# Kernel tuning notes

Measured on AMD Instinct MI355X. Metric: run time of the kernel, lower is better.

The kernel has to match this reference:

```python
import jax, jax.numpy as jnp
import numpy as np

OC, IC, KH, KW = 256, 128, 3, 3          # conv_weights_shape
S, R, Q = 16, 16, 16                      # n_subspaces, rank_transformations, rank_subspace
CTX = 256
HD, WD = OC * KH, IC * KW                 # dynamic_weights_shape = [768, 384]
ASYM = 1e-3
B = 32


def _make_index():
    # Faithful vectorization of DynamicConv2DMobius._create_index for the
    # non-inverted case (HD > WD): block_id = bi*nbj + bj over 3x3 tiles of the
    # [HD, WD] grid; tile goes to (out = block_id % OC, in = block_id // OC).
    base = np.arange(HD * WD).reshape(HD, WD)
    nbi, nbj = HD // KH, WD // KW          # == OC, IC here
    blocks = base.reshape(nbi, KH, nbj, KW).transpose(0, 2, 1, 3).reshape(nbi * nbj, KH, KW)
    # index[o, i] = blocks[i*OC + o]
    index = blocks.reshape(IC, OC, KH, KW).transpose(1, 0, 2, 3)
    return index.reshape(-1).astype(np.int32)  # flat gather map: conv.flat = dw.flat[idx]


def setup_inputs() -> dict:
    key = jax.random.key(0)
    ks = jax.random.split(key, 12)
    bconv_bound = 1.0 / np.sqrt(IC * KH * KW)
    return {
        "x": jax.random.normal(ks[0], (B, IC, 64, 64), jnp.float32),
        "context": jax.random.normal(ks[1], (B, CTX), jnp.float32),
        "W_mob": jax.random.normal(ks[2], (CTX, S, R, 8), jnp.float32) * 0.05,
        "z": jax.random.normal(ks[3], (S, R, 2), jnp.float32),
        "A_re": jax.random.normal(ks[4], (S, R, Q), jnp.float32) * 0.1,
        "A_im": jax.random.normal(ks[5], (S, R, Q), jnp.float32) * 0.1,
        "U": jax.random.normal(ks[6], (S, HD, Q), jnp.float32) * 0.05,
        "V": jax.random.normal(ks[7], (S, Q, WD), jnp.float32) * 0.05,
        "bias_dw": jax.random.uniform(ks[8], (HD, WD), jnp.float32, -ASYM, ASYM),
        "bias_conv": jax.random.uniform(ks[9], (OC,), jnp.float32, -bconv_bound, bconv_bound),
        "pad_val": jax.random.normal(ks[10], (1,), jnp.float32) * 1e-3,
        "offset_val": jax.random.normal(ks[11], (1,), jnp.float32) * 1e-3,
        "dw_index": jnp.asarray(_make_index()),
    }


def _forward(x, context, W_mob, z, A_re, A_im, U, V, bias_dw, bias_conv,
             pad_val, offset_val, dw_index):
    b = x.shape[0]
    # --- TensorComposerMobius: context -> per-sample Mobius coeffs -> low-rank weights
    m = jnp.einsum('bc,csrk->bsrk', context, W_mob)            # [B,S,R,8]
    a_re, a_im, b_re, b_im, c_re, c_im, d_re, d_im = [m[..., i] for i in range(8)]
    z_re, z_im = z[..., 0], z[..., 1]                           # [S,R]
    num_re = a_re * z_re - a_im * z_im + b_re
    num_im = a_re * z_im + a_im * z_re + b_im
    den_re = c_re * z_re - c_im * z_im + d_re
    den_im = c_re * z_im + c_im * z_re + d_im
    den2 = den_re * den_re + den_im * den_im + ASYM             # asymmetry regularizer
    w_re = (num_re * den_re + num_im * den_im) / den2
    w_im = (num_im * den_re - num_re * den_im) / den2
    s = jnp.einsum('bsr,srq->bsq', w_re, A_re) + jnp.einsum('bsr,srq->bsq', w_im, A_im)
    dw = jnp.einsum('bsq,shq,sqw->bhw', s, U, V)                # [B, 768, 384]
    dw = dw + bias_dw[None]                                     # bias_dynamic_weights_lib
    # --- block-gather into conv weight layout (torch.take with shifted index)
    conv_w = jnp.take(dw.reshape(b, -1), dw_index, axis=1).reshape(b, OC, IC, KH, KW)
    # --- dynamic padding value + dynamic offset
    xo = x + offset_val[0]
    hp, wp = x.shape[2] + 2, x.shape[3] + 2                     # padding [1,1,1,1]
    xp = jnp.full((b, IC, hp, wp), pad_val[0], x.dtype).at[:, :, 1:-1, 1:-1].set(xo)
    # --- per-sample conv2d (batched weights)
    def conv_one(xi, wi):
        return jax.lax.conv_general_dilated(
            xi[None], wi, window_strides=(1, 1), padding='VALID',
            rhs_dilation=(1, 1), dimension_numbers=('NCHW', 'OIHW', 'NCHW'))[0]
    out = jax.vmap(conv_one)(xp, conv_w)                        # [B, OC, 64, 64]
    return out + bias_conv[None, :, None, None]


def reference(x, context, W_mob, z, A_re, A_im, U, V, bias_dw, bias_conv,
              pad_val, offset_val, dw_index):
    return _forward(x, context, W_mob, z, A_re, A_im, U, V, bias_dw, bias_conv,
                    pad_val, offset_val, dw_index)
```

## Files before the change

kernel.cpp:

```cpp
#include <hip/hip_runtime.h>
#include <hip/hip_bf16.h>

typedef __attribute__((ext_vector_type(8))) short short8;
typedef __attribute__((ext_vector_type(4))) float f32x4;
typedef unsigned short u16;

#define B_      32
#define IC_     128
#define OC_     256
#define HD_     768
#define WD_     384
#define CTX_    256

static __device__ __forceinline__ u16 f2bf(float f) {
    union { float f; unsigned u; } x; x.f = f;
    unsigned r = x.u + 0x7FFFu + ((x.u >> 16) & 1u);
    return (u16)(r >> 16);
}

static __device__ __forceinline__ void glds16(const void* g, void* l) {
    __builtin_amdgcn_global_load_lds(
        (const __attribute__((address_space(1))) unsigned*)g,
        (__attribute__((address_space(3))) unsigned*)l, 16, 0, 0);
}

#define BARRIER() asm volatile("s_barrier" ::: "memory")
template <int N> static __device__ __forceinline__ void waitvm() {
    if constexpr (N == 0)      asm volatile("s_waitcnt vmcnt(0)" ::: "memory");
    else if constexpr (N == 4) asm volatile("s_waitcnt vmcnt(4)" ::: "memory");
    else if constexpr (N == 9) asm volatile("s_waitcnt vmcnt(9)" ::: "memory");
}

__global__ __launch_bounds__(256) void k1_mobius(
    const float* __restrict__ ctx, const float* __restrict__ Wm,
    const float* __restrict__ z, const float* __restrict__ Are,
    const float* __restrict__ Aim, float* __restrict__ sc) {
    int b = blockIdx.x, t = threadIdx.x;
    __shared__ float lctx[CTX_];
    __shared__ float lwre[256], lwim[256];
    lctx[t] = ctx[b * CTX_ + t];
    __syncthreads();
    float m0=0,m1=0,m2=0,m3=0,m4=0,m5=0,m6=0,m7=0;
    const float4* wp4 = (const float4*)Wm + (size_t)t * 2;
    #pragma unroll 4
    for (int c = 0; c < CTX_; ++c) {
        float4 w0 = wp4[(size_t)c * 512];
        float4 w1 = wp4[(size_t)c * 512 + 1];
        float cv = lctx[c];
        m0 += cv*w0.x; m1 += cv*w0.y; m2 += cv*w0.z; m3 += cv*w0.w;
        m4 += cv*w1.x; m5 += cv*w1.y; m6 += cv*w1.z; m7 += cv*w1.w;
    }
    float zre = z[t*2], zim = z[t*2+1];
    float nre = m0*zre - m1*zim + m2;
    float nim = m0*zim + m1*zre + m3;
    float dre = m4*zre - m5*zim + m6;
    float dim_ = m4*zim + m5*zre + m7;
    float den2 = dre*dre + dim_*dim_ + 1e-3f;
    lwre[t] = (nre*dre + nim*dim_) / den2;
    lwim[t] = (nim*dre - nre*dim_) / den2;
    __syncthreads();
    int s = t >> 4, q = t & 15;
    float acc = 0.f;
    #pragma unroll
    for (int r2 = 0; r2 < 16; ++r2) {
        int sr = s*16 + r2;
        acc += lwre[sr]*Are[sr*16 + q] + lwim[sr]*Aim[sr*16 + q];
    }
    sc[b*256 + t] = acc;
}

__global__ __launch_bounds__(256) void k2_pad(
    const float* __restrict__ x, const float* __restrict__ padv,
    const float* __restrict__ offv, u16* __restrict__ xp) {
    int yy = blockIdx.x, b = blockIdx.y, t = threadIdx.x;
    __shared__ u16 lds[64 * 136];
    float off = offv[0];
    u16 pb = f2bf(padv[0]);
    unsigned pp = (unsigned)pb | ((unsigned)pb << 16);
    int4 padvec = make_int4((int)pp, (int)pp, (int)pp, (int)pp);
    u16* row = xp + (size_t)(b * 66 + yy) * (66 * 128);
    if (yy == 0 || yy == 65) {
        for (int c = t; c < 1056; c += 256)
            *(int4*)(row + c * 8) = padvec;
        return;
    }
    int y = yy - 1;
    const float* xin = x + (size_t)b * 524288 + (size_t)y * 64;
    for (int id = t; id < 8192; id += 256) {
        int i = id >> 6, xx = id & 63;
        lds[xx * 136 + i] = f2bf(xin[(size_t)i * 4096 + xx] + off);
    }
    __syncthreads();
    for (int c = t; c < 1056; c += 256) {
        int e = c * 8, xx = e >> 7, i0 = e & 127;
        int4 v;
        if (xx == 0 || xx == 65) v = padvec;
        else v = *(const int4*)(lds + (xx - 1) * 136 + i0);
        *(int4*)(row + e) = v;
    }
}

__global__ __launch_bounds__(256) void k3_prep(
    const float* __restrict__ U, const float* __restrict__ V,
    u16* __restrict__ Ucat, float* __restrict__ Vt) {
    int id = blockIdx.x * 256 + threadIdx.x;
    if (id < 768 * 256) {
        int h = id >> 8, k = id & 255;
        int s = k >> 4, q = k & 15;
        Ucat[id] = f2bf(U[((size_t)s * HD_ + h) * 16 + q]);
    } else {
        int id2 = id - 768 * 256;
        int w = id2 >> 8, k = id2 & 255;
        Vt[id2] = V[(size_t)k * WD_ + w];
    }
}

__global__ __launch_bounds__(256, 2) void k4_dw(
    const u16* __restrict__ Ucat, const float* __restrict__ Vt,
    const float* __restrict__ sc, const float* __restrict__ bias_dw,
    u16* __restrict__ cw2) {
    int mt = blockIdx.x, khkw = blockIdx.y, b = blockIdx.z;
    int kh = khkw / 3, kw = khkw - kh * 3;
    int t = threadIdx.x;
    __shared__ __align__(16) u16 Al[128 * 40];
    __shared__ __align__(16) u16 Bl[128 * 40];
    __shared__ float scl[256];
    scl[t] = sc[b * 256 + t];
    f32x4 acc[4][4] = {};
    int wid = t >> 6, l = t & 63;
    int wm = wid >> 1, wn = wid & 1;
    int lr = l & 15, lg = l >> 4;
    int bi0 = mt * 128;
    for (int kc = 0; kc < 8; ++kc) {
        __syncthreads();
        #pragma unroll
        for (int it = 0; it < 2; ++it) {
            int cid = t + it * 256;
            int g = cid & 3, rr = cid >> 2;
            int4 v = *(const int4*)(Ucat + (size_t)((bi0 + rr) * 3 + kh) * 256 + kc * 32 + g * 8);
            *(int4*)(Al + rr * 40 + g * 8) = v;
        }
        #pragma unroll
        for (int it = 0; it < 4; ++it) {
            int cid = t + it * 256;
            int q = cid & 7, rr = cid >> 3;
            int kb = kc * 32 + q * 4;
            float4 v = *(const float4*)(Vt + (size_t)(rr * 3 + kw) * 256 + kb);
            ushort4 p;
            p.x = f2bf(v.x * scl[kb]);
            p.y = f2bf(v.y * scl[kb + 1]);
            p.z = f2bf(v.z * scl[kb + 2]);
            p.w = f2bf(v.w * scl[kb + 3]);
            *(ushort4*)(Bl + rr * 40 + q * 4) = p;
        }
        __syncthreads();
        short8 a[4];
        #pragma unroll
        for (int fm = 0; fm < 4; ++fm)
            a[fm] = *(const short8*)(Al + (wm * 64 + fm * 16 + lr) * 40 + lg * 8);
        #pragma unroll
        for (int fn = 0; fn < 4; ++fn) {
            short8 bb = *(const short8*)(Bl + (wn * 64 + fn * 16 + lr) * 40 + lg * 8);
            #pragma unroll
            for (int fm = 0; fm < 4; ++fm)
                acc[fm][fn] = __builtin_amdgcn_mfma_f32_16x16x32_bf16(a[fm], bb, acc[fm][fn], 0, 0, 0);
        }
    }
    u16* cwb = cw2 + (size_t)b * 294912;
    #pragma unroll
    for (int fm = 0; fm < 4; ++fm) {
        int i2 = mt * 8 + wm * 4 + fm;
        int B0 = bi0 + wm * 64 + fm * 16 + lg * 4;
        #pragma unroll
        for (int fn = 0; fn < 4; ++fn) {
            int bjj = wn * 64 + fn * 16 + lr;
            int wcol = bjj * 3 + kw;
            float v0 = acc[fm][fn][0] + bias_dw[(B0 + 0) * 3 * 384 + kh * 384 + wcol];
            float v2 = acc[fm][fn][2] + bias_dw[(B0 + 2) * 3 * 384 + kh * 384 + wcol];
            unsigned pe = (unsigned)f2bf(v0) | ((unsigned)f2bf(v2) << 16);
            size_t base = ((size_t)(khkw * 16 + i2) * 256);
            *(unsigned*)(cwb + (base + bjj) * 8 + 2 * lg) = pe;
            float v1 = acc[fm][fn][1] + bias_dw[(B0 + 1) * 3 * 384 + kh * 384 + wcol];
            float v3 = acc[fm][fn][3] + bias_dw[(B0 + 3) * 3 * 384 + kh * 384 + wcol];
            unsigned po = (unsigned)f2bf(v1) | ((unsigned)f2bf(v3) << 16);
            *(unsigned*)(cwb + (base + bjj + 128) * 8 + 2 * lg) = po;
        }
    }
}

static __device__ __forceinline__ void stage_W(
    const u16* cwb, int khkw, int ic, u16* wl, int t) {
    const u16* slice = cwb + ((size_t)(khkw * 16 + ic * 4) * 256) * 8;
    int wbase = t & ~63;
    #pragma unroll
    for (int it = 0; it < 4; ++it) {
        int cid = it * 256 + t;
        glds16(slice + (size_t)cid * 8, wl + (size_t)(it * 256 + wbase) * 8);
    }
}

static __device__ __forceinline__ void stage_X(
    const u16* xpb, int ic, int y0, u16* xl, int t) {
    int wbase = t & ~63;
    #pragma unroll
    for (int it = 0; it < 5; ++it) {
        int cid = it * 256 + t;
        const u16* g;
        if (cid < 1056) {
            int n = cid ^ ((cid >> 3) & 7);
            int gq = (n >= 792) ? 3 : (n >= 528) ? 2 : (n >= 264) ? 1 : 0;
            int rem = n - gq * 264;
            int r = (rem * 993) >> 16;
            int c = rem - r * 66;
            g = xpb + ((size_t)(y0 + r) * 66 + c) * 128 + ic * 32 + gq * 8;
        } else {
            g = xpb;
        }
        glds16(g, xl + (size_t)(it * 256 + wbase) * 8);
    }
}

__global__ __launch_bounds__(256, 2) void k6_conv(
    const u16* __restrict__ xp, const u16* __restrict__ cw2,
    const float* __restrict__ bias_conv, float* __restrict__ out) {
    int f = blockIdx.x;
    int xcd = f & 7, sub = f >> 3;
    int b = xcd * 4 + (sub >> 5);
    int nt = sub & 31;
    int t = threadIdx.x;
    int y0 = nt * 2;
    __shared__ __align__(16) u16 Wl[2][1024 * 8];
    __shared__ __align__(16) u16 Xl[2][1280 * 8];
    f32x4 acc[4][8] = {};
    int wid = t >> 6, l = t & 63, lr = l & 15, lg = l >> 4;
    const u16* xpb = xp + (size_t)b * (66 * 66 * 128);
    const u16* cwb = cw2 + (size_t)b * 294912;

    stage_X(xpb, 0, y0, Xl[0], t);
    stage_W(cwb, 0, 0, Wl[0], t);
    waitvm<0>();
    BARRIER();

    #pragma unroll
    for (int ic = 0; ic < 4; ++ic) {
        #pragma unroll
        for (int khkw = 0; khkw < 9; ++khkw) {
            const int s = ic * 9 + khkw;
            const int kh = khkw / 3, kw = khkw - kh * 3;
            if (khkw == 8 && ic < 3)
                stage_X(xpb, ic + 1, y0, Xl[(ic + 1) & 1], t);
            if (s + 1 < 36) {
                const int nk = (s + 1) % 9, nic = (s + 1) / 9;
                stage_W(cwb, nk, nic, Wl[(s + 1) & 1], t);
            }
            if (s == 35) waitvm<0>();
            else if (khkw == 8) waitvm<9>();
            else waitvm<4>();
            BARRIER();
            const u16* wl = Wl[s & 1];
            const u16* xl = Xl[ic & 1];
            short8 a[4];
            #pragma unroll
            for (int fm = 0; fm < 4; ++fm) {
                int o = wid * 64 + fm * 16 + lr;
                a[fm] = *(const short8*)(wl + (size_t)(lg * 256 + o) * 8);
            }
            __builtin_amdgcn_s_setprio(1);
            #pragma unroll
            for (int fn = 0; fn < 8; ++fn) {
                int r = (fn >> 2) + kh, c = (fn & 3) * 16 + lr + kw;
                int n = lg * 264 + r * 66 + c;
                int m = n ^ ((n >> 3) & 7);
                short8 bb = *(const short8*)(xl + (size_t)m * 8);
                #pragma unroll
                for (int fm = 0; fm < 4; ++fm)
                    acc[fm][fn] = __builtin_amdgcn_mfma_f32_16x16x32_bf16(a[fm], bb, acc[fm][fn], 0, 0, 0);
            }
            __builtin_amdgcn_s_setprio(0);
            if (s != 35) BARRIER();
        }
    }
    #pragma unroll
    for (int fm = 0; fm < 4; ++fm)
        #pragma unroll
        for (int fn = 0; fn < 8; ++fn) {
            int y = y0 + (fn >> 2);
            int xb = (fn & 3) * 16 + lr;
            #pragma unroll
            for (int j = 0; j < 4; ++j) {
                int o = wid * 64 + fm * 16 + lg * 4 + j;
                out[(((size_t)b * 256 + o) * 64 + y) * 64 + xb] = acc[fm][fn][j] + bias_conv[o];
            }
        }
}

extern "C" void kernel_launch(void* const* d_in, const int* in_sizes, int n_in,
                              void* d_out, int out_size, void* d_ws, size_t ws_size,
                              hipStream_t stream) {
    const float* x     = (const float*)d_in[0];
    const float* ctx   = (const float*)d_in[1];
    const float* Wm    = (const float*)d_in[2];
    const float* z     = (const float*)d_in[3];
    const float* Are   = (const float*)d_in[4];
    const float* Aim   = (const float*)d_in[5];
    const float* U     = (const float*)d_in[6];
    const float* V     = (const float*)d_in[7];
    const float* bdw   = (const float*)d_in[8];
    const float* bconv = (const float*)d_in[9];
    const float* padv  = (const float*)d_in[10];
    const float* offv  = (const float*)d_in[11];
    float* out = (float*)d_out;
    char* ws = (char*)d_ws;

    u16*   xp   = (u16*)(ws);
    u16*   cw2  = (u16*)(ws + 35684352);
    u16*   Ucat = (u16*)(ws + 54558720);
    float* Vt   = (float*)(ws + 54951936);
    float* sc   = (float*)(ws + 55345152);

    k1_mobius<<<32, 256, 0, stream>>>(ctx, Wm, z, Are, Aim, sc);
    k2_pad<<<dim3(66, 32), 256, 0, stream>>>(x, padv, offv, xp);
    k3_prep<<<1152, 256, 0, stream>>>(U, V, Ucat, Vt);
    k4_dw<<<dim3(2, 9, 32), 256, 0, stream>>>(Ucat, Vt, sc, bdw, cw2);
    k6_conv<<<1024, 256, 0, stream>>>(xp, cw2, bconv, out);
}
```

Measured before the change: 350.0 us.

## Load conv weights directly into registers and merge preprocessing kernels into one launch

The conv kernel stops staging weight slices through LDS with double buffering. Each lane now loads its MFMA A-fragments straight from global memory into a two-deep register ring, prefetched two steps ahead, which removes one LDS buffer and most per-step barriers. Barriers and vmcnt waits now happen only when the X tile changes, once per input-channel group. Separately, the mobius, pad and prep kernels are fused into one launch split by block index, saving launch overhead; in exchange the weight loads become uncoalesced 16-byte global reads per lane and register pressure rises.

```diff
diff --git a/kernel.cpp b/kernel.cpp
--- a/kernel.cpp
+++ b/kernel.cpp
@@ -25,93 +25,91 @@
 }
 
 #define BARRIER() asm volatile("s_barrier" ::: "memory")
-template <int N> static __device__ __forceinline__ void waitvm() {
-    if constexpr (N == 0)      asm volatile("s_waitcnt vmcnt(0)" ::: "memory");
-    else if constexpr (N == 4) asm volatile("s_waitcnt vmcnt(4)" ::: "memory");
-    else if constexpr (N == 9) asm volatile("s_waitcnt vmcnt(9)" ::: "memory");
-}
-
-__global__ __launch_bounds__(256) void k1_mobius(
+static __device__ __forceinline__ void waitvm0() {
+    asm volatile("s_waitcnt vmcnt(0)" ::: "memory");
+}
+
+__global__ __launch_bounds__(256) void k_pre(
     const float* __restrict__ ctx, const float* __restrict__ Wm,
     const float* __restrict__ z, const float* __restrict__ Are,
-    const float* __restrict__ Aim, float* __restrict__ sc) {
-    int b = blockIdx.x, t = threadIdx.x;
-    __shared__ float lctx[CTX_];
-    __shared__ float lwre[256], lwim[256];
-    lctx[t] = ctx[b * CTX_ + t];
-    __syncthreads();
-    float m0=0,m1=0,m2=0,m3=0,m4=0,m5=0,m6=0,m7=0;
-    const float4* wp4 = (const float4*)Wm + (size_t)t * 2;
-    #pragma unroll 4
-    for (int c = 0; c < CTX_; ++c) {
-        float4 w0 = wp4[(size_t)c * 512];
-        float4 w1 = wp4[(size_t)c * 512 + 1];
-        float cv = lctx[c];
-        m0 += cv*w0.x; m1 += cv*w0.y; m2 += cv*w0.z; m3 += cv*w0.w;
-        m4 += cv*w1.x; m5 += cv*w1.y; m6 += cv*w1.z; m7 += cv*w1.w;
-    }
-    float zre = z[t*2], zim = z[t*2+1];
-    float nre = m0*zre - m1*zim + m2;
-    float nim = m0*zim + m1*zre + m3;
-    float dre = m4*zre - m5*zim + m6;
-    float dim_ = m4*zim + m5*zre + m7;
-    float den2 = dre*dre + dim_*dim_ + 1e-3f;
-    lwre[t] = (nre*dre + nim*dim_) / den2;
-    lwim[t] = (nim*dre - nre*dim_) / den2;
-    __syncthreads();
-    int s = t >> 4, q = t & 15;
-    float acc = 0.f;
-    #pragma unroll
-    for (int r2 = 0; r2 < 16; ++r2) {
-        int sr = s*16 + r2;
-        acc += lwre[sr]*Are[sr*16 + q] + lwim[sr]*Aim[sr*16 + q];
-    }
-    sc[b*256 + t] = acc;
-}
-
-__global__ __launch_bounds__(256) void k2_pad(
-    const float* __restrict__ x, const float* __restrict__ padv,
-    const float* __restrict__ offv, u16* __restrict__ xp) {
-    int yy = blockIdx.x, b = blockIdx.y, t = threadIdx.x;
-    __shared__ u16 lds[64 * 136];
-    float off = offv[0];
-    u16 pb = f2bf(padv[0]);
-    unsigned pp = (unsigned)pb | ((unsigned)pb << 16);
-    int4 padvec = make_int4((int)pp, (int)pp, (int)pp, (int)pp);
-    u16* row = xp + (size_t)(b * 66 + yy) * (66 * 128);
-    if (yy == 0 || yy == 65) {
-        for (int c = t; c < 1056; c += 256)
-            *(int4*)(row + c * 8) = padvec;
-        return;
-    }
-    int y = yy - 1;
-    const float* xin = x + (size_t)b * 524288 + (size_t)y * 64;
-    for (int id = t; id < 8192; id += 256) {
-        int i = id >> 6, xx = id & 63;
-        lds[xx * 136 + i] = f2bf(xin[(size_t)i * 4096 + xx] + off);
-    }
-    __syncthreads();
-    for (int c = t; c < 1056; c += 256) {
-        int e = c * 8, xx = e >> 7, i0 = e & 127;
-        int4 v;
-        if (xx == 0 || xx == 65) v = padvec;
-        else v = *(const int4*)(lds + (xx - 1) * 136 + i0);
-        *(int4*)(row + e) = v;
-    }
-}
-
-__global__ __launch_bounds__(256) void k3_prep(
+    const float* __restrict__ Aim, const float* __restrict__ x,
+    const float* __restrict__ padv, const float* __restrict__ offv,
     const float* __restrict__ U, const float* __restrict__ V,
+    float* __restrict__ sc, u16* __restrict__ xp,
     u16* __restrict__ Ucat, float* __restrict__ Vt) {
-    int id = blockIdx.x * 256 + threadIdx.x;
-    if (id < 768 * 256) {
-        int h = id >> 8, k = id & 255;
-        int s = k >> 4, q = k & 15;
-        Ucat[id] = f2bf(U[((size_t)s * HD_ + h) * 16 + q]);
+    int bid = blockIdx.x, t = threadIdx.x;
+    if (bid < 32) {
+        int b = bid;
+        __shared__ float lctx[CTX_];
+        __shared__ float lwre[256], lwim[256];
+        lctx[t] = ctx[b * CTX_ + t];
+        __syncthreads();
+        float m0=0,m1=0,m2=0,m3=0,m4=0,m5=0,m6=0,m7=0;
+        const float4* wp4 = (const float4*)Wm + (size_t)t * 2;
+        #pragma unroll 4
+        for (int c = 0; c < CTX_; ++c) {
+            float4 w0 = wp4[(size_t)c * 512];
+            float4 w1 = wp4[(size_t)c * 512 + 1];
+            float cv = lctx[c];
+            m0 += cv*w0.x; m1 += cv*w0.y; m2 += cv*w0.z; m3 += cv*w0.w;
+            m4 += cv*w1.x; m5 += cv*w1.y; m6 += cv*w1.z; m7 += cv*w1.w;
+        }
+        float zre = z[t*2], zim = z[t*2+1];
+        float nre = m0*zre - m1*zim + m2;
+        float nim = m0*zim + m1*zre + m3;
+        float dre = m4*zre - m5*zim + m6;
+        float dim_ = m4*zim + m5*zre + m7;
+        float den2 = dre*dre + dim_*dim_ + 1e-3f;
+        lwre[t] = (nre*dre + nim*dim_) / den2;
+        lwim[t] = (nim*dre - nre*dim_) / den2;
+        __syncthreads();
+        int s = t >> 4, q = t & 15;
+        float acc = 0.f;
+        #pragma unroll
+        for (int r2 = 0; r2 < 16; ++r2) {
+            int sr = s*16 + r2;
+            acc += lwre[sr]*Are[sr*16 + q] + lwim[sr]*Aim[sr*16 + q];
+        }
+        sc[b*256 + t] = acc;
+    } else if (bid < 2144) {
+        int pb_ = bid - 32;
+        int yy = pb_ % 66, b = pb_ / 66;
+        __shared__ u16 lds[64 * 136];
+        float off = offv[0];
+        u16 pb = f2bf(padv[0]);
+        unsigned pp = (unsigned)pb | ((unsigned)pb << 16);
+        int4 padvec = make_int4((int)pp, (int)pp, (int)pp, (int)pp);
+        u16* row = xp + (size_t)(b * 66 + yy) * (66 * 128);
+        if (yy == 0 || yy == 65) {
+            for (int c = t; c < 1056; c += 256)
+                *(int4*)(row + c * 8) = padvec;
+            return;
+        }
+        int y = yy - 1;
+        const float* xin = x + (size_t)b * 524288 + (size_t)y * 64;
+        for (int id = t; id < 8192; id += 256) {
+            int i = id >> 6, xx = id & 63;
+            lds[xx * 136 + i] = f2bf(xin[(size_t)i * 4096 + xx] + off);
+        }
+        __syncthreads();
+        for (int c = t; c < 1056; c += 256) {
+            int e = c * 8, xx = e >> 7, i0 = e & 127;
+            int4 v;
+            if (xx == 0 || xx == 65) v = padvec;
+            else v = *(const int4*)(lds + (xx - 1) * 136 + i0);
+            *(int4*)(row + e) = v;
+        }
     } else {
-        int id2 = id - 768 * 256;
-        int w = id2 >> 8, k = id2 & 255;
-        Vt[id2] = V[(size_t)k * WD_ + w];
+        int id = (bid - 2144) * 256 + t;
+        if (id < 768 * 256) {
+            int h = id >> 8, k = id & 255;
+            int s = k >> 4, q = k & 15;
+            Ucat[id] = f2bf(U[((size_t)s * HD_ + h) * 16 + q]);
+        } else {
+            int id2 = id - 768 * 256;
+            int w = id2 >> 8, k = id2 & 255;
+            Vt[id2] = V[(size_t)k * WD_ + w];
+        }
     }
 }
 
@@ -188,17 +186,6 @@
     }
 }
 
-static __device__ __forceinline__ void stage_W(
-    const u16* cwb, int khkw, int ic, u16* wl, int t) {
-    const u16* slice = cwb + ((size_t)(khkw * 16 + ic * 4) * 256) * 8;
-    int wbase = t & ~63;
-    #pragma unroll
-    for (int it = 0; it < 4; ++it) {
-        int cid = it * 256 + t;
-        glds16(slice + (size_t)cid * 8, wl + (size_t)(it * 256 + wbase) * 8);
-    }
-}
-
 static __device__ __forceinline__ void stage_X(
     const u16* xpb, int ic, int y0, u16* xl, int t) {
     int wbase = t & ~63;
@@ -229,17 +216,21 @@
     int nt = sub & 31;
     int t = threadIdx.x;
     int y0 = nt * 2;
-    __shared__ __align__(16) u16 Wl[2][1024 * 8];
     __shared__ __align__(16) u16 Xl[2][1280 * 8];
     f32x4 acc[4][8] = {};
     int wid = t >> 6, l = t & 63, lr = l & 15, lg = l >> 4;
     const u16* xpb = xp + (size_t)b * (66 * 66 * 128);
     const u16* cwb = cw2 + (size_t)b * 294912;
-
+    const u16* wbase = cwb + (size_t)((lg * 256) + wid * 64 + lr) * 8;
+
+    short8 wreg[2][4];
     stage_X(xpb, 0, y0, Xl[0], t);
-    stage_W(cwb, 0, 0, Wl[0], t);
-    waitvm<0>();
-    BARRIER();
+    #pragma unroll
+    for (int fm = 0; fm < 4; ++fm)
+        wreg[0][fm] = *(const short8*)(wbase + ((size_t)(0 * 16) * 256 + fm * 16) * 8);
+    #pragma unroll
+    for (int fm = 0; fm < 4; ++fm)
+        wreg[1][fm] = *(const short8*)(wbase + ((size_t)(1 * 16) * 256 + fm * 16) * 8);
 
     #pragma unroll
     for (int ic = 0; ic < 4; ++ic) {
@@ -247,24 +238,13 @@
         for (int khkw = 0; khkw < 9; ++khkw) {
             const int s = ic * 9 + khkw;
             const int kh = khkw / 3, kw = khkw - kh * 3;
-            if (khkw == 8 && ic < 3)
-                stage_X(xpb, ic + 1, y0, Xl[(ic + 1) & 1], t);
-            if (s + 1 < 36) {
-                const int nk = (s + 1) % 9, nic = (s + 1) / 9;
-                stage_W(cwb, nk, nic, Wl[(s + 1) & 1], t);
+            if (khkw == 0) {
+                waitvm0();
+                __builtin_amdgcn_sched_barrier(0);
+                BARRIER();
+                if (ic < 3) stage_X(xpb, ic + 1, y0, Xl[(ic + 1) & 1], t);
             }
-            if (s == 35) waitvm<0>();
-            else if (khkw == 8) waitvm<9>();
-            else waitvm<4>();
-            BARRIER();
-            const u16* wl = Wl[s & 1];
             const u16* xl = Xl[ic & 1];
-            short8 a[4];
-            #pragma unroll
-            for (int fm = 0; fm < 4; ++fm) {
-                int o = wid * 64 + fm * 16 + lr;
-                a[fm] = *(const short8*)(wl + (size_t)(lg * 256 + o) * 8);
-            }
             __builtin_amdgcn_s_setprio(1);
             #pragma unroll
             for (int fn = 0; fn < 8; ++fn) {
@@ -274,10 +254,15 @@
                 short8 bb = *(const short8*)(xl + (size_t)m * 8);
                 #pragma unroll
                 for (int fm = 0; fm < 4; ++fm)
-                    acc[fm][fn] = __builtin_amdgcn_mfma_f32_16x16x32_bf16(a[fm], bb, acc[fm][fn], 0, 0, 0);
+                    acc[fm][fn] = __builtin_amdgcn_mfma_f32_16x16x32_bf16(wreg[s & 1][fm], bb, acc[fm][fn], 0, 0, 0);
             }
             __builtin_amdgcn_s_setprio(0);
-            if (s != 35) BARRIER();
+            if (s + 2 < 36) {
+                const int s2 = s + 2, nic = s2 / 9, nk = s2 % 9;
+                #pragma unroll
+                for (int fm = 0; fm < 4; ++fm)
+                    wreg[s & 1][fm] = *(const short8*)(wbase + ((size_t)(nk * 16 + nic * 4) * 256 + fm * 16) * 8);
+            }
         }
     }
     #pragma unroll
@@ -318,9 +303,8 @@
     float* Vt   = (float*)(ws + 54951936);
     float* sc   = (float*)(ws + 55345152);
 
-    k1_mobius<<<32, 256, 0, stream>>>(ctx, Wm, z, Are, Aim, sc);
-    k2_pad<<<dim3(66, 32), 256, 0, stream>>>(x, padv, offv, xp);
-    k3_prep<<<1152, 256, 0, stream>>>(U, V, Ucat, Vt);
+    k_pre<<<3296, 256, 0, stream>>>(ctx, Wm, z, Are, Aim, x, padv, offv, U, V,
+                                    sc, xp, Ucat, Vt);
     k4_dw<<<dim3(2, 9, 32), 256, 0, stream>>>(Ucat, Vt, sc, bdw, cw2);
     k6_conv<<<1024, 256, 0, stream>>>(xp, cw2, bconv, out);
 }
```

Measured after the change: 331.4 us. -5.3%, faster.
